# Performance work log

Measured on AMD Instinct MI355X. Metric: run time of the kernel, lower is better.

## Reference

```python
import jax, jax.numpy as jnp
import numpy as np

V, D, L, H, HKV, E = 32000, 1024, 4, 16, 4, 4
HD = D // H
B, T = 2, 1024
EPS = 1e-6
ROPE_BASE = 10000.0


def setup_inputs() -> dict:
    key = jax.random.key(0)
    ks = jax.random.split(key, 9)
    s = 0.02
    return {
        "input_ids": jax.random.randint(ks[0], (B, T), 0, V),
        "token_emb": jax.random.normal(ks[1], (V, D), jnp.float32) * s,
        "ln1_w": jnp.ones((L, D), jnp.float32),
        "q_w": jax.random.normal(ks[2], (L, D, D), jnp.float32) * s,
        "k_w": jax.random.normal(ks[3], (L, HKV * HD, D), jnp.float32) * s,
        "v_w": jax.random.normal(ks[4], (L, HKV * HD, D), jnp.float32) * s,
        "o_w": jax.random.normal(ks[5], (L, D, D), jnp.float32) * s,
        "ln2_w": jnp.ones((L, D), jnp.float32),
        "w1_w": jax.random.normal(ks[6], (L, E * D, D), jnp.float32) * s,
        "w2_w": jax.random.normal(ks[7], (L, D, E * D), jnp.float32) * s,
        "w3_w": jax.random.normal(ks[8], (L, E * D, D), jnp.float32) * s,
        "lnf_w": jnp.ones((D,), jnp.float32),
    }


def rmsnorm(x, w):
    var = jnp.mean(x * x, axis=-1, keepdims=True)
    return w * (x * jax.lax.rsqrt(var + EPS))


def rope_tables(t, dtype):
    inv_freq = 1.0 / (ROPE_BASE ** (jnp.arange(0, HD, 2, dtype=jnp.float32) / HD))
    freqs = jnp.outer(jnp.arange(t, dtype=jnp.float32), inv_freq)  # [T, HD/2]
    emb = jnp.concatenate([freqs, freqs], axis=-1)  # [T, HD]
    return emb.astype(dtype)[None, None], None  # placeholder shape helper


def rotate_half(x):
    x1, x2 = x[..., : HD // 2], x[..., HD // 2 :]
    return jnp.concatenate([-x2, x1], axis=-1)


def block(x, cos, sin, ln1, wq, wk, wv, wo, ln2, w1, w2, w3):
    # attention (pre-norm)
    h = rmsnorm(x, ln1)
    q = jnp.einsum('btd,ed->bte', h, wq).reshape(B, T, H, HD).transpose(0, 2, 1, 3)
    k = jnp.einsum('btd,ed->bte', h, wk).reshape(B, T, HKV, HD).transpose(0, 2, 1, 3)
    v = jnp.einsum('btd,ed->bte', h, wv).reshape(B, T, HKV, HD).transpose(0, 2, 1, 3)
    q = q * cos + rotate_half(q) * sin
    k = k * cos + rotate_half(k) * sin
    # GQA: repeat kv heads (repeat_interleave semantics)
    g = H // HKV
    k = jnp.repeat(k, g, axis=1)
    v = jnp.repeat(v, g, axis=1)
    scale = 1.0 / np.sqrt(HD)
    scores = jnp.einsum('bhqd,bhkd->bhqk', q, k) * scale
    causal = jnp.triu(jnp.ones((T, T), jnp.bool_), k=1)[None, None]
    scores = jnp.where(causal, -jnp.inf, scores)
    attn = jax.nn.softmax(scores.astype(jnp.float32), axis=-1).astype(q.dtype)
    o = jnp.einsum('bhqk,bhkd->bhqd', attn, v)
    o = o.transpose(0, 2, 1, 3).reshape(B, T, D)
    x = x + jnp.einsum('btd,ed->bte', o, wo)
    # SwiGLU FFN
    h = rmsnorm(x, ln2)
    gate = jax.nn.silu(jnp.einsum('btd,fd->btf', h, w1))
    up = jnp.einsum('btd,fd->btf', h, w3)
    x = x + jnp.einsum('btf,df->btd', gate * up, w2)
    return x


def forward(input_ids, token_emb, ln1_w, q_w, k_w, v_w, o_w, ln2_w, w1_w, w2_w, w3_w, lnf_w):
    x = token_emb[input_ids]  # [B,T,D]
    inv_freq = 1.0 / (ROPE_BASE ** (jnp.arange(0, HD, 2, dtype=jnp.float32) / HD))
    freqs = jnp.outer(jnp.arange(T, dtype=jnp.float32), inv_freq)
    emb = jnp.concatenate([freqs, freqs], axis=-1)  # [T, HD]
    cos = jnp.cos(emb)[None, None]  # [1,1,T,HD]
    sin = jnp.sin(emb)[None, None]
    for i in range(L):
        x = block(x, cos, sin, ln1_w[i], q_w[i], k_w[i], v_w[i], o_w[i],
                  ln2_w[i], w1_w[i], w2_w[i], w3_w[i])
    x = rmsnorm(x, lnf_w)
    logits = jnp.einsum('btd,vd->btv', x, token_emb)  # tied lm_head
    return logits


def reference(input_ids, token_emb, ln1_w, q_w, k_w, v_w, o_w, ln2_w, w1_w, w2_w, w3_w, lnf_w):
    return forward(input_ids, token_emb, ln1_w, q_w, k_w, v_w, o_w, ln2_w, w1_w, w2_w, w3_w, lnf_w)
```

## Files before the change

### kernel.cpp

```cpp
#include <hip/hip_runtime.h>
#include <math.h>

#define TT 1024
#define BB 2
#define DD 1024
#define NH 16
#define NKV 4
#define HD 64
#define ED 4096
#define LL 4
#define VV 32000
#define QKVS 1536

typedef __bf16 bf16x8 __attribute__((ext_vector_type(8)));
typedef float f32x4 __attribute__((ext_vector_type(4)));

__device__ inline unsigned short f2bf(float f) {
  unsigned u = __float_as_uint(f);
  u += 0x7fffu + ((u >> 16) & 1u);
  return (unsigned short)(u >> 16);
}

#define GLL16(gsrc, ldst)                                                            \
  __builtin_amdgcn_global_load_lds((const __attribute__((address_space(1))) void*)(gsrc), \
                                   (__attribute__((address_space(3))) void*)(ldst), 16, 0, 0)

__global__ void convw_kernel(const float* __restrict__ src, unsigned short* __restrict__ dst) {
  size_t i = (size_t)blockIdx.x * blockDim.x + threadIdx.x;
  float4 v = ((const float4*)src)[i];
  uint2 o;
  o.x = f2bf(v.x) | ((unsigned)f2bf(v.y) << 16);
  o.y = f2bf(v.z) | ((unsigned)f2bf(v.w) << 16);
  ((uint2*)dst)[i] = o;
}

__global__ void conv_qkv_kernel(const float* __restrict__ qw, const float* __restrict__ kw,
                                const float* __restrict__ vw, unsigned short* __restrict__ dst) {
  size_t i = (size_t)blockIdx.x * blockDim.x + threadIdx.x;
  size_t e = i * 4;
  int l = (int)(e / (QKVS * 1024));
  int rem = (int)(e - (size_t)l * (QKVS * 1024));
  int row = rem >> 10;
  int col = rem & 1023;
  const float* src;
  if (row < 1024) src = qw + (((size_t)l << 20) + ((size_t)row << 10)) + col;
  else if (row < 1280) src = kw + (((size_t)l << 18) + ((size_t)(row - 1024) << 10)) + col;
  else src = vw + (((size_t)l << 18) + ((size_t)(row - 1280) << 10)) + col;
  float4 v = *(const float4*)src;
  uint2 o;
  o.x = f2bf(v.x) | ((unsigned)f2bf(v.y) << 16);
  o.y = f2bf(v.z) | ((unsigned)f2bf(v.w) << 16);
  ((uint2*)dst)[i] = o;
}

__global__ void conv_w13_kernel(const float* __restrict__ w1, const float* __restrict__ w3,
                                unsigned short* __restrict__ dst) {
  size_t i = (size_t)blockIdx.x * blockDim.x + threadIdx.x;
  size_t e = i * 4;
  int l = (int)(e >> 23);
  int rem = (int)(e & ((1u << 23) - 1));
  int row = rem >> 10;
  int col = rem & 1023;
  const float* src;
  if (row < 4096) src = w1 + (((size_t)l << 22) + ((size_t)row << 10)) + col;
  else src = w3 + (((size_t)l << 22) + ((size_t)(row - 4096) << 10)) + col;
  float4 v = *(const float4*)src;
  uint2 o;
  o.x = f2bf(v.x) | ((unsigned)f2bf(v.y) << 16);
  o.y = f2bf(v.z) | ((unsigned)f2bf(v.w) << 16);
  ((uint2*)dst)[i] = o;
}

__global__ void embed_kernel(const int* __restrict__ ids, const float* __restrict__ emb,
                             float* __restrict__ x) {
  int row = blockIdx.x;
  int id = ids[row];
  const float4* src = (const float4*)(emb + (size_t)id * DD);
  float4* dst = (float4*)(x + (size_t)row * DD);
  dst[threadIdx.x] = src[threadIdx.x];
}

__global__ __launch_bounds__(256) void rmsnorm_kernel(const float* __restrict__ x,
                                                      const float* __restrict__ wgt,
                                                      unsigned short* __restrict__ out) {
  int row = blockIdx.x;
  int tid = threadIdx.x;
  float4 v = *(const float4*)(x + (size_t)row * DD + tid * 4);
  float ss = v.x * v.x + v.y * v.y + v.z * v.z + v.w * v.w;
#pragma unroll
  for (int off = 32; off >= 1; off >>= 1) ss += __shfl_xor(ss, off);
  __shared__ float part[4];
  if ((tid & 63) == 0) part[tid >> 6] = ss;
  __syncthreads();
  ss = part[0] + part[1] + part[2] + part[3];
  float sc = rsqrtf(ss * (1.0f / DD) + 1e-6f);
  float4 wv = *(const float4*)(wgt + tid * 4);
  uint2 o;
  o.x = f2bf(v.x * wv.x * sc) | ((unsigned)f2bf(v.y * wv.y * sc) << 16);
  o.y = f2bf(v.z * wv.z * sc) | ((unsigned)f2bf(v.w * wv.w * sc) << 16);
  *(uint2*)(out + (size_t)row * DD + tid * 4) = o;
}

template <int EPI>
__global__ __launch_bounds__(256) void gemm_bb(const unsigned short* __restrict__ A,
                                               const unsigned short* __restrict__ W,
                                               float* __restrict__ C, int M, int N, int K) {
  __shared__ unsigned short As[128 * 32];
  __shared__ unsigned short Bs[128 * 32];
  const int tid = threadIdx.x;
  const int lane = tid & 63;
  const int w = tid >> 6;
  const int wm = (w >> 1) * 64;
  const int wn = (w & 1) * 64;
  const int l15 = lane & 15;
  const int quad = lane >> 4;
  const int q8 = quad * 8;

  const int nby = gridDim.y;
  const int nwg = gridDim.x * nby;
  int orig = blockIdx.x * nby + blockIdx.y;
  int swz = orig;
  if ((nwg & 7) == 0) {
    int cpx = nwg >> 3;
    swz = (orig & 7) * cpx + (orig >> 3);
  }
  const int mBase = (swz % nby) * 128;
  const int nBase = (swz / nby) * 128;

  const unsigned short* Ab = A + (size_t)mBase * K;
  const unsigned short* Wb = W + (size_t)nBase * K;
  const int r0 = tid >> 2;
  const int c8 = (tid & 3) * 8;

  f32x4 acc[4][4] = {};

  for (int kt = 0; kt < K; kt += 32) {
    __syncthreads();
    GLL16(Ab + (size_t)r0 * K + kt + c8, As + (w * 64) * 8);
    GLL16(Ab + (size_t)(r0 + 64) * K + kt + c8, As + (256 + w * 64) * 8);
    GLL16(Wb + (size_t)r0 * K + kt + c8, Bs + (w * 64) * 8);
    GLL16(Wb + (size_t)(r0 + 64) * K + kt + c8, Bs + (256 + w * 64) * 8);
    __syncthreads();
    bf16x8 af[4], bfv[4];
#pragma unroll
    for (int ms = 0; ms < 4; ms++)
      af[ms] = *(const bf16x8*)&As[(wm + ms * 16 + l15) * 32 + q8];
#pragma unroll
    for (int ns = 0; ns < 4; ns++)
      bfv[ns] = *(const bf16x8*)&Bs[(wn + ns * 16 + l15) * 32 + q8];
#pragma unroll
    for (int ms = 0; ms < 4; ms++)
#pragma unroll
      for (int ns = 0; ns < 4; ns++)
        acc[ms][ns] = __builtin_amdgcn_mfma_f32_16x16x32_bf16(af[ms], bfv[ns], acc[ms][ns], 0, 0, 0);
  }
#pragma unroll
  for (int ms = 0; ms < 4; ms++)
#pragma unroll
    for (int ns = 0; ns < 4; ns++)
#pragma unroll
      for (int r = 0; r < 4; r++) {
        int row = mBase + wm + ms * 16 + quad * 4 + r;
        int col = nBase + wn + ns * 16 + l15;
        size_t idx = (size_t)row * N + col;
        if (EPI == 0) C[idx] = acc[ms][ns][r];
        else C[idx] += acc[ms][ns][r];
      }
}

template <int EPI>
__global__ __launch_bounds__(256) void gemm_bt(const unsigned short* __restrict__ A,
                                               const float* __restrict__ W,
                                               float* __restrict__ C, int M, int N, int K) {
  __shared__ unsigned short As[128 * 40];
  __shared__ unsigned short Bs[128 * 40];
  const int tid = threadIdx.x;
  const int lane = tid & 63;
  const int w = tid >> 6;
  const int wm = (w >> 1) * 64;
  const int wn = (w & 1) * 64;
  const int l15 = lane & 15;
  const int quad = lane >> 4;
  const int q8 = quad * 8;

  const int nby = gridDim.y;
  const int nwg = gridDim.x * nby;
  int orig = blockIdx.x * nby + blockIdx.y;
  int swz = orig;
  if ((nwg & 7) == 0) {
    int cpx = nwg >> 3;
    swz = (orig & 7) * cpx + (orig >> 3);
  }
  const int mBase = (swz % nby) * 128;
  const int nBase = (swz / nby) * 128;

  f32x4 acc[4][4] = {};

  for (int kt = 0; kt < K; kt += 32) {
    __syncthreads();
#pragma unroll
    for (int i = 0; i < 2; i++) {
      int chunk = tid + 256 * i;
      int r = chunk >> 2, c8 = (chunk & 3) * 8;
      uint4 v = *(const uint4*)(A + (size_t)(mBase + r) * K + kt + c8);
      *(uint4*)&As[r * 40 + c8] = v;
    }
#pragma unroll
    for (int i = 0; i < 2; i++) {
      int chunk = tid + 256 * i;
      int r = chunk >> 2, c8 = (chunk & 3) * 8;
      const float4* wp = (const float4*)(W + (size_t)(nBase + r) * K + kt + c8);
      float4 f0 = wp[0], f1 = wp[1];
      uint4 v;
      v.x = f2bf(f0.x) | ((unsigned)f2bf(f0.y) << 16);
      v.y = f2bf(f0.z) | ((unsigned)f2bf(f0.w) << 16);
      v.z = f2bf(f1.x) | ((unsigned)f2bf(f1.y) << 16);
      v.w = f2bf(f1.z) | ((unsigned)f2bf(f1.w) << 16);
      *(uint4*)&Bs[r * 40 + c8] = v;
    }
    __syncthreads();
    bf16x8 af[4], bfv[4];
#pragma unroll
    for (int ms = 0; ms < 4; ms++)
      af[ms] = *(const bf16x8*)&As[(wm + ms * 16 + l15) * 40 + q8];
#pragma unroll
    for (int ns = 0; ns < 4; ns++)
      bfv[ns] = *(const bf16x8*)&Bs[(wn + ns * 16 + l15) * 40 + q8];
#pragma unroll
    for (int ms = 0; ms < 4; ms++)
#pragma unroll
      for (int ns = 0; ns < 4; ns++)
        acc[ms][ns] = __builtin_amdgcn_mfma_f32_16x16x32_bf16(af[ms], bfv[ns], acc[ms][ns], 0, 0, 0);
  }
#pragma unroll
  for (int ms = 0; ms < 4; ms++)
#pragma unroll
    for (int ns = 0; ns < 4; ns++)
#pragma unroll
      for (int r = 0; r < 4; r++) {
        int row = mBase + wm + ms * 16 + quad * 4 + r;
        int col = nBase + wn + ns * 16 + l15;
        size_t idx = (size_t)row * N + col;
        if (EPI == 0) C[idx] = acc[ms][ns][r];
        else C[idx] += acc[ms][ns][r];
      }
}

__global__ void rope_kernel(float* __restrict__ buf, int nh, int stride) {
  int e = blockIdx.x * blockDim.x + threadIdx.x;
  int per_row = nh * 32;
  int row = e / per_row;
  int rem = e - row * per_row;
  int hh = rem >> 5;
  int d = rem & 31;
  int t = row & (TT - 1);
  float invf = __expf(-(float)d * 0.28782313662f);
  float ang = (float)t * invf;
  float sv, cv;
  sincosf(ang, &sv, &cv);
  float* p = buf + (size_t)row * stride + hh * 64 + d;
  float x1 = p[0], x2 = p[32];
  p[0] = x1 * cv - x2 * sv;
  p[32] = x2 * cv + x1 * sv;
}

__global__ __launch_bounds__(256) void attn_fwd(const float* __restrict__ Q,
                                                const float* __restrict__ Kb,
                                                const float* __restrict__ Vb,
                                                unsigned short* __restrict__ O) {
  __shared__ unsigned short Qs[64 * 72];
  __shared__ unsigned short Ks[64 * 72];
  __shared__ unsigned short Vt[64 * 72];
  const int tid = threadIdx.x;
  const int lane = tid & 63;
  const int w = tid >> 6;
  const int l15 = lane & 15;
  const int quad = lane >> 4;
  const int q8 = quad * 8;
  const int bh = blockIdx.x;
  const int b = bh / NH, h = bh % NH;
  const int hkv = h >> 2;
  const int qb = blockIdx.y;

#pragma unroll
  for (int i = 0; i < 4; i++) {
    int cc = tid + 256 * i;
    int r = cc >> 4, d4 = (cc & 15) * 4;
    float4 v = *(const float4*)(Q + (size_t)(b * TT + qb * 64 + r) * QKVS + h * HD + d4);
    uint2 p;
    p.x = f2bf(v.x) | ((unsigned)f2bf(v.y) << 16);
    p.y = f2bf(v.z) | ((unsigned)f2bf(v.w) << 16);
    *(uint2*)&Qs[r * 72 + d4] = p;
  }
  __syncthreads();
  bf16x8 qa0 = *(const bf16x8*)&Qs[(w * 16 + l15) * 72 + q8];
  bf16x8 qa1 = *(const bf16x8*)&Qs[(w * 16 + l15) * 72 + 32 + q8];

  f32x4 oacc[4] = {};
  float m_i[4], l_i[4];
#pragma unroll
  for (int r = 0; r < 4; r++) { m_i[r] = -1e30f; l_i[r] = 0.f; }

  for (int kb = 0; kb <= qb; kb++) {
    __syncthreads();
#pragma unroll
    for (int i = 0; i < 4; i++) {
      int cc = tid + 256 * i;
      int r = cc >> 4, d4 = (cc & 15) * 4;
      size_t grow = (size_t)(b * TT + kb * 64 + r) * QKVS + hkv * HD + d4;
      float4 kv = *(const float4*)(Kb + grow);
      uint2 p;
      p.x = f2bf(kv.x) | ((unsigned)f2bf(kv.y) << 16);
      p.y = f2bf(kv.z) | ((unsigned)f2bf(kv.w) << 16);
      *(uint2*)&Ks[r * 72 + d4] = p;
      float4 vv = *(const float4*)(Vb + grow);
      Vt[(d4 + 0) * 72 + r] = f2bf(vv.x);
      Vt[(d4 + 1) * 72 + r] = f2bf(vv.y);
      Vt[(d4 + 2) * 72 + r] = f2bf(vv.z);
      Vt[(d4 + 3) * 72 + r] = f2bf(vv.w);
    }
    __syncthreads();
    f32x4 s[4];
#pragma unroll
    for (int ns = 0; ns < 4; ns++) {
      bf16x8 k0 = *(const bf16x8*)&Ks[(ns * 16 + l15) * 72 + q8];
      bf16x8 k1 = *(const bf16x8*)&Ks[(ns * 16 + l15) * 72 + 32 + q8];
      f32x4 z = {};
      z = __builtin_amdgcn_mfma_f32_16x16x32_bf16(qa0, k0, z, 0, 0, 0);
      s[ns] = __builtin_amdgcn_mfma_f32_16x16x32_bf16(qa1, k1, z, 0, 0, 0);
    }
#pragma unroll
    for (int ns = 0; ns < 4; ns++)
#pragma unroll
      for (int r = 0; r < 4; r++) {
        float sv = s[ns][r] * 0.125f;
        if (kb == qb) {
          int qloc = w * 16 + quad * 4 + r;
          int kloc = ns * 16 + l15;
          if (kloc > qloc) sv = -1e30f;
        }
        s[ns][r] = sv;
      }
    float p[4][4];
    float alpha[4];
#pragma unroll
    for (int r = 0; r < 4; r++) {
      float mx = fmaxf(fmaxf(s[0][r], s[1][r]), fmaxf(s[2][r], s[3][r]));
#pragma unroll
      for (int off = 1; off < 16; off <<= 1) mx = fmaxf(mx, __shfl_xor(mx, off));
      float mnew = fmaxf(m_i[r], mx);
      alpha[r] = __expf(m_i[r] - mnew);
      float rs = 0.f;
#pragma unroll
      for (int ns = 0; ns < 4; ns++) {
        p[ns][r] = __expf(s[ns][r] - mnew);
        rs += p[ns][r];
      }
#pragma unroll
      for (int off = 1; off < 16; off <<= 1) rs += __shfl_xor(rs, off);
      l_i[r] = l_i[r] * alpha[r] + rs;
      m_i[r] = mnew;
    }
#pragma unroll
    for (int ds = 0; ds < 4; ds++)
#pragma unroll
      for (int r = 0; r < 4; r++) oacc[ds][r] *= alpha[r];
#pragma unroll
    for (int ns = 0; ns < 4; ns++)
#pragma unroll
      for (int r = 0; r < 4; r++)
        Qs[(w * 16 + quad * 4 + r) * 72 + ns * 16 + l15] = f2bf(p[ns][r]);
    __syncthreads();
    bf16x8 pa0 = *(const bf16x8*)&Qs[(w * 16 + l15) * 72 + q8];
    bf16x8 pa1 = *(const bf16x8*)&Qs[(w * 16 + l15) * 72 + 32 + q8];
#pragma unroll
    for (int ds = 0; ds < 4; ds++) {
      bf16x8 v0 = *(const bf16x8*)&Vt[(ds * 16 + l15) * 72 + q8];
      bf16x8 v1 = *(const bf16x8*)&Vt[(ds * 16 + l15) * 72 + 32 + q8];
      oacc[ds] = __builtin_amdgcn_mfma_f32_16x16x32_bf16(pa0, v0, oacc[ds], 0, 0, 0);
      oacc[ds] = __builtin_amdgcn_mfma_f32_16x16x32_bf16(pa1, v1, oacc[ds], 0, 0, 0);
    }
  }
#pragma unroll
  for (int ds = 0; ds < 4; ds++)
#pragma unroll
    for (int r = 0; r < 4; r++) {
      int row = qb * 64 + w * 16 + quad * 4 + r;
      int col = h * HD + ds * 16 + l15;
      O[(size_t)(b * TT + row) * DD + col] = f2bf(oacc[ds][r] / l_i[r]);
    }
}

__global__ void swiglu_kernel(const float* __restrict__ G, unsigned short* __restrict__ out) {
  size_t i = (size_t)blockIdx.x * blockDim.x + threadIdx.x;
  size_t i4 = i * 4;
  int row = (int)(i4 >> 12);
  int col = (int)(i4 & 4095);
  float4 g = *(const float4*)(G + (size_t)row * 8192 + col);
  float4 u = *(const float4*)(G + (size_t)row * 8192 + 4096 + col);
  float r0 = g.x / (1.f + __expf(-g.x)) * u.x;
  float r1 = g.y / (1.f + __expf(-g.y)) * u.y;
  float r2 = g.z / (1.f + __expf(-g.z)) * u.z;
  float r3 = g.w / (1.f + __expf(-g.w)) * u.w;
  uint2 o;
  o.x = f2bf(r0) | ((unsigned)f2bf(r1) << 16);
  o.y = f2bf(r2) | ((unsigned)f2bf(r3) << 16);
  ((uint2*)out)[i] = o;
}

extern "C" void kernel_launch(void* const* d_in, const int* in_sizes, int n_in,
                              void* d_out, int out_size, void* d_ws, size_t ws_size,
                              hipStream_t stream) {
  const int* ids = (const int*)d_in[0];
  const float* emb = (const float*)d_in[1];
  const float* ln1 = (const float*)d_in[2];
  const float* qw = (const float*)d_in[3];
  const float* kw = (const float*)d_in[4];
  const float* vw = (const float*)d_in[5];
  const float* ow = (const float*)d_in[6];
  const float* ln2 = (const float*)d_in[7];
  const float* w1 = (const float*)d_in[8];
  const float* w2 = (const float*)d_in[9];
  const float* w3 = (const float*)d_in[10];
  const float* lnf = (const float*)d_in[11];

  const int BT = BB * TT;
  const size_t MB = 1024ull * 1024ull;
  char* ob = (char*)d_out;

  float* guf = (float*)ob;
  unsigned short* hb2 = (unsigned short*)(ob + 64 * MB);
  unsigned short* qkvb = (unsigned short*)(ob + 80 * MB);
  unsigned short* owb = (unsigned short*)(ob + 92 * MB);
  unsigned short* w13b = (unsigned short*)(ob + 100 * MB);
  unsigned short* w2b = (unsigned short*)(ob + 164 * MB);

  char* wb = (char*)d_ws;
  unsigned short* hb = (unsigned short*)wb;
  float* x;
  float* qkv;
  unsigned short* ao;
  if (ws_size >= 28 * MB) {
    x = (float*)(wb + 4 * MB);
    qkv = (float*)(wb + 12 * MB);
    ao = (unsigned short*)(wb + 24 * MB);
  } else {
    x = (float*)(ob + 196 * MB);
    qkv = (float*)(ob + 204 * MB);
    ao = (unsigned short*)(ob + 216 * MB);
  }
  const bool bf16_logits = (ws_size >= 92 * MB);
  unsigned short* embb = bf16_logits ? (unsigned short*)(wb + 28 * MB) : nullptr;

  conv_qkv_kernel<<<6144, 256, 0, stream>>>(qw, kw, vw, qkvb);
  convw_kernel<<<4096, 256, 0, stream>>>(ow, owb);
  conv_w13_kernel<<<32768, 256, 0, stream>>>(w1, w3, w13b);
  convw_kernel<<<16384, 256, 0, stream>>>(w2, w2b);
  if (bf16_logits) convw_kernel<<<32000, 256, 0, stream>>>(emb, embb);

  embed_kernel<<<BT, 256, 0, stream>>>(ids, emb, x);
  for (int l = 0; l < LL; l++) {
    rmsnorm_kernel<<<BT, 256, 0, stream>>>(x, ln1 + l * DD, hb);
    gemm_bb<0><<<dim3(QKVS / 128, BT / 128), 256, 0, stream>>>(
        hb, qkvb + (size_t)l * QKVS * DD, qkv, BT, QKVS, DD);
    rope_kernel<<<(BT * NH * 32) / 256, 256, 0, stream>>>(qkv, NH, QKVS);
    rope_kernel<<<(BT * NKV * 32) / 256, 256, 0, stream>>>(qkv + 1024, NKV, QKVS);
    attn_fwd<<<dim3(BB * NH, TT / 64), 256, 0, stream>>>(qkv, qkv + 1024, qkv + 1280, ao);
    gemm_bb<1><<<dim3(DD / 128, BT / 128), 256, 0, stream>>>(
        ao, owb + (size_t)l * DD * DD, x, BT, DD, DD);
    rmsnorm_kernel<<<BT, 256, 0, stream>>>(x, ln2 + l * DD, hb);
    gemm_bb<0><<<dim3((2 * ED) / 128, BT / 128), 256, 0, stream>>>(
        hb, w13b + (size_t)l * 2 * ED * DD, guf, BT, 2 * ED, DD);
    swiglu_kernel<<<(BT * ED / 4) / 256, 256, 0, stream>>>(guf, hb2);
    gemm_bb<1><<<dim3(DD / 128, BT / 128), 256, 0, stream>>>(
        hb2, w2b + (size_t)l * DD * ED, x, BT, DD, ED);
  }
  rmsnorm_kernel<<<BT, 256, 0, stream>>>(x, lnf, hb);
  if (bf16_logits) {
    gemm_bb<0><<<dim3(VV / 128, BT / 128), 256, 0, stream>>>(hb, embb, (float*)d_out, BT, VV, DD);
  } else {
    gemm_bt<0><<<dim3(VV / 128, BT / 128), 256, 0, stream>>>(hb, emb, (float*)d_out, BT, VV, DD);
  }
}
```

Before: 2.032 ms.

## Fuse SwiGLU into gate/up GEMM epilogue and split-K the down projection

The w1/w3 weights are interleaved in 16-row groups during conversion, so each GEMM tile holds matching gate and up columns. The tile can then apply SiLU(g)*u in its epilogue and write bf16 directly, removing the fp32 gate/up buffer and the separate swiglu pass. The down projection now uses split-K over two z slices writing fp32 partials, followed by an add kernel that accumulates both into the residual. The block-index swizzle order also changes. The cost is an extra partial-sum buffer and an extra pass over it.

```diff
diff --git a/kernel.cpp b/kernel.cpp
--- a/kernel.cpp
+++ b/kernel.cpp
@@ -59,11 +59,12 @@
   size_t e = i * 4;
   int l = (int)(e >> 23);
   int rem = (int)(e & ((1u << 23) - 1));
-  int row = rem >> 10;
+  int r = rem >> 10;
   int col = rem & 1023;
-  const float* src;
-  if (row < 4096) src = w1 + (((size_t)l << 22) + ((size_t)row << 10)) + col;
-  else src = w3 + (((size_t)l << 22) + ((size_t)(row - 4096) << 10)) + col;
+  int grp = r >> 4;
+  int f = (grp >> 1) * 16 + (r & 15);
+  const float* base = (grp & 1) ? w3 : w1;
+  const float* src = base + (((size_t)l << 22) + ((size_t)f << 10)) + col;
   float4 v = *(const float4*)src;
   uint2 o;
   o.x = f2bf(v.x) | ((unsigned)f2bf(v.y) << 16);
@@ -101,10 +102,22 @@
   *(uint2*)(out + (size_t)row * DD + tid * 4) = o;
 }
 
+__global__ void add2_kernel(float* __restrict__ x, const float* __restrict__ p0,
+                            const float* __restrict__ p1) {
+  size_t i = (size_t)blockIdx.x * blockDim.x + threadIdx.x;
+  float4 a = ((const float4*)x)[i];
+  float4 b = ((const float4*)p0)[i];
+  float4 c = ((const float4*)p1)[i];
+  a.x += b.x + c.x; a.y += b.y + c.y; a.z += b.z + c.z; a.w += b.w + c.w;
+  ((float4*)x)[i] = a;
+}
+
 template <int EPI>
 __global__ __launch_bounds__(256) void gemm_bb(const unsigned short* __restrict__ A,
                                                const unsigned short* __restrict__ W,
-                                               float* __restrict__ C, int M, int N, int K) {
+                                               float* __restrict__ C,
+                                               unsigned short* __restrict__ O2,
+                                               int M, int N, int K) {
   __shared__ unsigned short As[128 * 32];
   __shared__ unsigned short Bs[128 * 32];
   const int tid = threadIdx.x;
@@ -118,14 +131,18 @@
 
   const int nby = gridDim.y;
   const int nwg = gridDim.x * nby;
-  int orig = blockIdx.x * nby + blockIdx.y;
-  int swz = orig;
+  const int bid = blockIdx.y * gridDim.x + blockIdx.x;
+  int wk = bid;
   if ((nwg & 7) == 0) {
     int cpx = nwg >> 3;
-    swz = (orig & 7) * cpx + (orig >> 3);
-  }
-  const int mBase = (swz % nby) * 128;
-  const int nBase = (swz / nby) * 128;
+    wk = (bid & 7) * cpx + (bid >> 3);
+  }
+  const int mBase = (wk % nby) * 128;
+  const int nBase = (wk / nby) * 128;
+
+  const int ksl = K / gridDim.z;
+  const int kb0 = blockIdx.z * ksl;
+  if (EPI == 0) C += (size_t)blockIdx.z * M * N;
 
   const unsigned short* Ab = A + (size_t)mBase * K;
   const unsigned short* Wb = W + (size_t)nBase * K;
@@ -134,7 +151,7 @@
 
   f32x4 acc[4][4] = {};
 
-  for (int kt = 0; kt < K; kt += 32) {
+  for (int kt = kb0; kt < kb0 + ksl; kt += 32) {
     __syncthreads();
     GLL16(Ab + (size_t)r0 * K + kt + c8, As + (w * 64) * 8);
     GLL16(Ab + (size_t)(r0 + 64) * K + kt + c8, As + (256 + w * 64) * 8);
@@ -154,18 +171,36 @@
       for (int ns = 0; ns < 4; ns++)
         acc[ms][ns] = __builtin_amdgcn_mfma_f32_16x16x32_bf16(af[ms], bfv[ns], acc[ms][ns], 0, 0, 0);
   }
-#pragma unroll
-  for (int ms = 0; ms < 4; ms++)
-#pragma unroll
-    for (int ns = 0; ns < 4; ns++)
+
+  if (EPI == 2) {
+    const int fBase = ((nBase + wn) >> 5) * 16;
+#pragma unroll
+    for (int ms = 0; ms < 4; ms++)
 #pragma unroll
       for (int r = 0; r < 4; r++) {
         int row = mBase + wm + ms * 16 + quad * 4 + r;
-        int col = nBase + wn + ns * 16 + l15;
-        size_t idx = (size_t)row * N + col;
-        if (EPI == 0) C[idx] = acc[ms][ns][r];
-        else C[idx] += acc[ms][ns][r];
+#pragma unroll
+        for (int pp = 0; pp < 2; pp++) {
+          float g = acc[ms][pp * 2][r];
+          float u = acc[ms][pp * 2 + 1][r];
+          float res = g / (1.f + __expf(-g)) * u;
+          O2[(size_t)row * ED + fBase + pp * 16 + l15] = f2bf(res);
+        }
       }
+  } else {
+#pragma unroll
+    for (int ms = 0; ms < 4; ms++)
+#pragma unroll
+      for (int ns = 0; ns < 4; ns++)
+#pragma unroll
+        for (int r = 0; r < 4; r++) {
+          int row = mBase + wm + ms * 16 + quad * 4 + r;
+          int col = nBase + wn + ns * 16 + l15;
+          size_t idx = (size_t)row * N + col;
+          if (EPI == 0) C[idx] = acc[ms][ns][r];
+          else C[idx] += acc[ms][ns][r];
+        }
+  }
 }
 
 template <int EPI>
@@ -185,14 +220,14 @@
 
   const int nby = gridDim.y;
   const int nwg = gridDim.x * nby;
-  int orig = blockIdx.x * nby + blockIdx.y;
-  int swz = orig;
+  const int bid = blockIdx.y * gridDim.x + blockIdx.x;
+  int wk = bid;
   if ((nwg & 7) == 0) {
     int cpx = nwg >> 3;
-    swz = (orig & 7) * cpx + (orig >> 3);
-  }
-  const int mBase = (swz % nby) * 128;
-  const int nBase = (swz / nby) * 128;
+    wk = (bid & 7) * cpx + (bid >> 3);
+  }
+  const int mBase = (wk % nby) * 128;
+  const int nBase = (wk / nby) * 128;
 
   f32x4 acc[4][4] = {};
 
@@ -201,22 +236,22 @@
 #pragma unroll
     for (int i = 0; i < 2; i++) {
       int chunk = tid + 256 * i;
-      int r = chunk >> 2, c8 = (chunk & 3) * 8;
-      uint4 v = *(const uint4*)(A + (size_t)(mBase + r) * K + kt + c8);
-      *(uint4*)&As[r * 40 + c8] = v;
+      int r = chunk >> 2, cc8 = (chunk & 3) * 8;
+      uint4 v = *(const uint4*)(A + (size_t)(mBase + r) * K + kt + cc8);
+      *(uint4*)&As[r * 40 + cc8] = v;
     }
 #pragma unroll
     for (int i = 0; i < 2; i++) {
       int chunk = tid + 256 * i;
-      int r = chunk >> 2, c8 = (chunk & 3) * 8;
-      const float4* wp = (const float4*)(W + (size_t)(nBase + r) * K + kt + c8);
+      int r = chunk >> 2, cc8 = (chunk & 3) * 8;
+      const float4* wp = (const float4*)(W + (size_t)(nBase + r) * K + kt + cc8);
       float4 f0 = wp[0], f1 = wp[1];
       uint4 v;
       v.x = f2bf(f0.x) | ((unsigned)f2bf(f0.y) << 16);
       v.y = f2bf(f0.z) | ((unsigned)f2bf(f0.w) << 16);
       v.z = f2bf(f1.x) | ((unsigned)f2bf(f1.y) << 16);
       v.w = f2bf(f1.z) | ((unsigned)f2bf(f1.w) << 16);
-      *(uint4*)&Bs[r * 40 + c8] = v;
+      *(uint4*)&Bs[r * 40 + cc8] = v;
     }
     __syncthreads();
     bf16x8 af[4], bfv[4];
@@ -391,23 +426,6 @@
     }
 }
 
-__global__ void swiglu_kernel(const float* __restrict__ G, unsigned short* __restrict__ out) {
-  size_t i = (size_t)blockIdx.x * blockDim.x + threadIdx.x;
-  size_t i4 = i * 4;
-  int row = (int)(i4 >> 12);
-  int col = (int)(i4 & 4095);
-  float4 g = *(const float4*)(G + (size_t)row * 8192 + col);
-  float4 u = *(const float4*)(G + (size_t)row * 8192 + 4096 + col);
-  float r0 = g.x / (1.f + __expf(-g.x)) * u.x;
-  float r1 = g.y / (1.f + __expf(-g.y)) * u.y;
-  float r2 = g.z / (1.f + __expf(-g.z)) * u.z;
-  float r3 = g.w / (1.f + __expf(-g.w)) * u.w;
-  uint2 o;
-  o.x = f2bf(r0) | ((unsigned)f2bf(r1) << 16);
-  o.y = f2bf(r2) | ((unsigned)f2bf(r3) << 16);
-  ((uint2*)out)[i] = o;
-}
-
 extern "C" void kernel_launch(void* const* d_in, const int* in_sizes, int n_in,
                               void* d_out, int out_size, void* d_ws, size_t ws_size,
                               hipStream_t stream) {
@@ -459,25 +477,27 @@
   if (bf16_logits) convw_kernel<<<32000, 256, 0, stream>>>(emb, embb);
 
   embed_kernel<<<BT, 256, 0, stream>>>(ids, emb, x);
+  float* p0 = guf;
+  float* p1 = guf + (size_t)BT * DD;
   for (int l = 0; l < LL; l++) {
     rmsnorm_kernel<<<BT, 256, 0, stream>>>(x, ln1 + l * DD, hb);
     gemm_bb<0><<<dim3(QKVS / 128, BT / 128), 256, 0, stream>>>(
-        hb, qkvb + (size_t)l * QKVS * DD, qkv, BT, QKVS, DD);
+        hb, qkvb + (size_t)l * QKVS * DD, qkv, nullptr, BT, QKVS, DD);
     rope_kernel<<<(BT * NH * 32) / 256, 256, 0, stream>>>(qkv, NH, QKVS);
     rope_kernel<<<(BT * NKV * 32) / 256, 256, 0, stream>>>(qkv + 1024, NKV, QKVS);
     attn_fwd<<<dim3(BB * NH, TT / 64), 256, 0, stream>>>(qkv, qkv + 1024, qkv + 1280, ao);
     gemm_bb<1><<<dim3(DD / 128, BT / 128), 256, 0, stream>>>(
-        ao, owb + (size_t)l * DD * DD, x, BT, DD, DD);
+        ao, owb + (size_t)l * DD * DD, x, nullptr, BT, DD, DD);
     rmsnorm_kernel<<<BT, 256, 0, stream>>>(x, ln2 + l * DD, hb);
-    gemm_bb<0><<<dim3((2 * ED) / 128, BT / 128), 256, 0, stream>>>(
-        hb, w13b + (size_t)l * 2 * ED * DD, guf, BT, 2 * ED, DD);
-    swiglu_kernel<<<(BT * ED / 4) / 256, 256, 0, stream>>>(guf, hb2);
-    gemm_bb<1><<<dim3(DD / 128, BT / 128), 256, 0, stream>>>(
-        hb2, w2b + (size_t)l * DD * ED, x, BT, DD, ED);
+    gemm_bb<2><<<dim3((2 * ED) / 128, BT / 128), 256, 0, stream>>>(
+        hb, w13b + (size_t)l * 2 * ED * DD, nullptr, hb2, BT, 2 * ED, DD);
+    gemm_bb<0><<<dim3(DD / 128, BT / 128, 2), 256, 0, stream>>>(
+        hb2, w2b + (size_t)l * DD * ED, p0, nullptr, BT, DD, ED);
+    add2_kernel<<<(BT * DD / 4) / 256, 256, 0, stream>>>(x, p0, p1);
   }
   rmsnorm_kernel<<<BT, 256, 0, stream>>>(x, lnf, hb);
   if (bf16_logits) {
-    gemm_bb<0><<<dim3(VV / 128, BT / 128), 256, 0, stream>>>(hb, embb, (float*)d_out, BT, VV, DD);
+    gemm_bb<0><<<dim3(VV / 128, BT / 128), 256, 0, stream>>>(hb, embb, (float*)d_out, nullptr, BT, VV, DD);
   } else {
     gemm_bt<0><<<dim3(VV / 128, BT / 128), 256, 0, stream>>>(hb, emb, (float*)d_out, BT, VV, DD);
   }
```

Result: faster. 1.845 ms (-9.2%).
